# Kernel optimization log

Measured on AMD Instinct MI355X. Metric: run time of the kernel, lower is better.

Reference implementation:

```python
import jax, jax.numpy as jnp
import numpy as np

B, S, H = 4, 1024, 2048
NQ, NKV, D = 32, 4, 128
EPS = 1e-6
THETA = 1e6


def setup_inputs() -> dict:
    key = jax.random.key(0)
    k1, k2, k3 = jax.random.split(key, 3)
    hidden = jax.random.normal(k1, (B, S, H), jnp.float32) * 0.02
    w_qkv = jax.random.normal(k2, (H, (NQ + 2 * NKV) * D), jnp.float32) * 0.02
    w_o = jax.random.normal(k3, (NQ * D, H), jnp.float32) * 0.02
    q_norm_w = jnp.ones((D,), jnp.float32)
    k_norm_w = jnp.ones((D,), jnp.float32)
    # rotary tables, broadcast to [B, S, D]
    inv_freq = 1.0 / (THETA ** (jnp.arange(0, D, 2, dtype=jnp.float32) / D))
    freqs = jnp.arange(S, dtype=jnp.float32)[:, None] * inv_freq[None, :]  # [S, D/2]
    emb = jnp.concatenate([freqs, freqs], axis=-1)  # [S, D]
    cos = jnp.broadcast_to(jnp.cos(emb)[None], (B, S, D))
    sin = jnp.broadcast_to(jnp.sin(emb)[None], (B, S, D))
    return {"hidden": hidden, "w_qkv": w_qkv, "w_o": w_o,
            "q_norm_w": q_norm_w, "k_norm_w": k_norm_w, "cos": cos, "sin": sin}


def _rms_norm(x, w):
    xf = x.astype(jnp.float32)
    var = jnp.mean(xf * xf, axis=-1, keepdims=True)
    return (w * (xf * jax.lax.rsqrt(var + EPS))).astype(x.dtype)


def _rotate_half(x):
    h = x.shape[-1] // 2
    return jnp.concatenate([-x[..., h:], x[..., :h]], axis=-1)


def reference(hidden, w_qkv, w_o, q_norm_w, k_norm_w, cos, sin):
    b, s, _ = hidden.shape
    qkv = jnp.einsum('bsh,he->bse', hidden, w_qkv)
    q = qkv[..., : NQ * D].reshape(b, s, NQ, D)
    k = qkv[..., NQ * D: (NQ + NKV) * D].reshape(b, s, NKV, D)
    v = qkv[..., (NQ + NKV) * D:].reshape(b, s, NKV, D)

    # per-head RMSNorm on Q and K
    q = _rms_norm(q, q_norm_w)
    k = _rms_norm(k, k_norm_w)

    # fused RoPE (rotate-half), cos/sin broadcast over heads
    c = cos[:, :, None, :]
    sn = sin[:, :, None, :]
    q = q * c + _rotate_half(q) * sn
    k = k * c + _rotate_half(k) * sn

    # GQA causal flash-attention (prefill, sparse_mode=3 -> causal)
    g = NQ // NKV
    qg = q.reshape(b, s, NKV, g, D)
    scale = 1.0 / jnp.sqrt(jnp.asarray(D, hidden.dtype))
    scores = jnp.einsum('bqkgd,bskd->bkgqs', qg, k) * scale  # [B,NKV,g,S,S]
    causal = jnp.tril(jnp.ones((s, s), bool))
    scores = jnp.where(causal[None, None, None], scores, jnp.finfo(scores.dtype).min)
    probs = jax.nn.softmax(scores, axis=-1)
    out = jnp.einsum('bkgqs,bskd->bqkgd', probs, v).reshape(b, s, NQ * D)
    return jnp.einsum('bse,eh->bsh', out, w_o)
```

## Files before the change

### kernel.cpp

```cpp
#include <hip/hip_runtime.h>

#define BB 4
#define SS 1024
#define HH 2048
#define NQH 32
#define NKVH 4
#define DD 128
#define EQKV 5120

typedef __attribute__((ext_vector_type(8))) short s8v;
typedef __attribute__((ext_vector_type(4))) short s4v;
typedef __attribute__((ext_vector_type(4))) float f4v;

__device__ __forceinline__ unsigned short f2bf(float f) {
  unsigned int u = __builtin_bit_cast(unsigned int, f);
  u += 0x7fffu + ((u >> 16) & 1u);
  return (unsigned short)(u >> 16);
}
__device__ __forceinline__ float bf2f(unsigned short s) {
  unsigned int u = ((unsigned int)s) << 16;
  return __builtin_bit_cast(float, u);
}

__device__ __forceinline__ void async16(unsigned short* lds, const unsigned short* g) {
  __builtin_amdgcn_global_load_lds(
      (const __attribute__((address_space(1))) unsigned int*)g,
      (__attribute__((address_space(3))) unsigned int*)lds, 16, 0, 0);
}


__global__ __launch_bounds__(256) void cvt_bf16(const float* __restrict__ in,
                                                unsigned short* __restrict__ out, int n) {
  int i = (blockIdx.x * 256 + threadIdx.x) * 4;
  if (i >= n) return;
  f4v v = *reinterpret_cast<const f4v*>(in + i);
  s4v o;
#pragma unroll
  for (int j = 0; j < 4; ++j) o[j] = (short)f2bf(v[j]);
  *reinterpret_cast<s4v*>(out + i) = o;
}

__global__ __launch_bounds__(256) void transpose_cvt(const float* __restrict__ in,
                                                     unsigned short* __restrict__ out,
                                                     int K, int N) {
  __shared__ unsigned short T[64][65];
  const int k0 = blockIdx.y * 64, n0 = blockIdx.x * 64;
  const int t = threadIdx.x;
  const int r = t >> 4, c4 = (t & 15) * 4;
#pragma unroll
  for (int i = 0; i < 4; ++i) {
    f4v v = *reinterpret_cast<const f4v*>(&in[(size_t)(k0 + r + i * 16) * N + n0 + c4]);
#pragma unroll
    for (int j = 0; j < 4; ++j) T[r + i * 16][c4 + j] = f2bf(v[j]);
  }
  __syncthreads();
#pragma unroll
  for (int i = 0; i < 4; ++i) {
    int n = r + i * 16;
    s4v o;
#pragma unroll
    for (int j = 0; j < 4; ++j) o[j] = (short)T[c4 + j][n];
    *reinterpret_cast<s4v*>(&out[(size_t)(n0 + n) * K + k0 + c4]) = o;
  }
}

__global__ __launch_bounds__(256) void vtrans(const unsigned short* __restrict__ qkv,
                                              unsigned short* __restrict__ Vt) {
  __shared__ unsigned short T[64][68];
  const int s0 = blockIdx.x * 64;
  const int d0 = blockIdx.y * 64;
  const int bk = blockIdx.z;
  const int b = bk >> 2, hkv = bk & 3;
  const int t = threadIdx.x;
  const int r = t >> 4, c4 = (t & 15) * 4;
  const unsigned short* src = qkv + (size_t)(b * SS + s0) * EQKV + (NQH + NKVH + hkv) * DD + d0;
#pragma unroll
  for (int i = 0; i < 4; ++i) {
    int s = r + i * 16;
    s4v v = *reinterpret_cast<const s4v*>(src + (size_t)s * EQKV + c4);
    *reinterpret_cast<s4v*>(&T[s][c4]) = v;
  }
  __syncthreads();
#pragma unroll
  for (int i = 0; i < 4; ++i) {
    int d = r + i * 16;
    s4v o;
#pragma unroll
    for (int j = 0; j < 4; ++j) o[j] = (short)T[c4 + j][d];
    *reinterpret_cast<s4v*>(&Vt[((size_t)bk * DD + d0 + d) * SS + s0 + c4]) = o;
  }
}

template <bool CF32>
__global__ __launch_bounds__(512) void gemm_deep(const unsigned short* __restrict__ A,
                                                 const unsigned short* __restrict__ Bt,
                                                 void* __restrict__ Cp,
                                                 int M, int N, int K, int lda) {
  __shared__ unsigned short RING[6][12288];
  const int tid = threadIdx.x;
  const int ln = tid & 63, w = tid >> 6;
  const int la = ln & 15, quad = ln >> 4;
  const int wr = w >> 2, wc = w & 3;

  const int G = gridDim.x, cpx = G >> 3;
  const int swz = (blockIdx.x & 7) * cpx + (blockIdx.x >> 3);
  const int ytiles = M >> 7;
  const int by = swz % ytiles, bx = swz / ytiles;
  const int m0 = by * 128, n0 = bx * 256;

  f4v acc[4][4] = {};

  const int srow = tid >> 2;
  const int schunk = (tid & 3) ^ ((tid >> 3) & 3);
  const int rb0 = w * 32 + (ln >> 2);
  const unsigned short* pA  = A  + (size_t)(m0 + srow) * lda + schunk * 8;
  const unsigned short* pB0 = Bt + (size_t)(n0 + rb0) * K   + schunk * 8;
  const unsigned short* pB1 = pB0 + (size_t)16 * K;
  unsigned short* ldsA = nullptr;

  const int fch = (quad ^ ((la >> 1) & 3)) * 8;
  const int ar = (wr * 64 + la) * 32;
  const int br = 4096 + (wc * 64 + la) * 32;

#define STAGE(s, koff)                                          \
  async16(&RING[s][w * 512], pA + (koff));                      \
  async16(&RING[s][4096 + w * 1024], pB0 + (koff));             \
  async16(&RING[s][4096 + w * 1024 + 512], pB1 + (koff));

#pragma unroll
  for (int pp = 0; pp < 5; ++pp) { STAGE(pp, pp * 32) }
  asm volatile("s_waitcnt vmcnt(12)" ::: "memory");
  __builtin_amdgcn_s_barrier();

  const int NP = K >> 5;
  const int kend = K - 32;
  int u = 0, su = 5, ks = 160;
  for (int p = 0; p < NP; ++p) {
    s8v a0 = *reinterpret_cast<const s8v*>(&RING[u][ar + fch]);
    s8v a1 = *reinterpret_cast<const s8v*>(&RING[u][ar + 512 + fch]);
    s8v a2 = *reinterpret_cast<const s8v*>(&RING[u][ar + 1024 + fch]);
    s8v a3 = *reinterpret_cast<const s8v*>(&RING[u][ar + 1536 + fch]);
    s8v b0 = *reinterpret_cast<const s8v*>(&RING[u][br + fch]);
    s8v b1 = *reinterpret_cast<const s8v*>(&RING[u][br + 512 + fch]);
    s8v b2 = *reinterpret_cast<const s8v*>(&RING[u][br + 1024 + fch]);
    s8v b3 = *reinterpret_cast<const s8v*>(&RING[u][br + 1536 + fch]);
    STAGE(su, ks)
    __builtin_amdgcn_s_setprio(1);
    acc[0][0] = __builtin_amdgcn_mfma_f32_16x16x32_bf16(a0, b0, acc[0][0], 0, 0, 0);
    acc[0][1] = __builtin_amdgcn_mfma_f32_16x16x32_bf16(a0, b1, acc[0][1], 0, 0, 0);
    acc[0][2] = __builtin_amdgcn_mfma_f32_16x16x32_bf16(a0, b2, acc[0][2], 0, 0, 0);
    acc[0][3] = __builtin_amdgcn_mfma_f32_16x16x32_bf16(a0, b3, acc[0][3], 0, 0, 0);
    acc[1][0] = __builtin_amdgcn_mfma_f32_16x16x32_bf16(a1, b0, acc[1][0], 0, 0, 0);
    acc[1][1] = __builtin_amdgcn_mfma_f32_16x16x32_bf16(a1, b1, acc[1][1], 0, 0, 0);
    acc[1][2] = __builtin_amdgcn_mfma_f32_16x16x32_bf16(a1, b2, acc[1][2], 0, 0, 0);
    acc[1][3] = __builtin_amdgcn_mfma_f32_16x16x32_bf16(a1, b3, acc[1][3], 0, 0, 0);
    acc[2][0] = __builtin_amdgcn_mfma_f32_16x16x32_bf16(a2, b0, acc[2][0], 0, 0, 0);
    acc[2][1] = __builtin_amdgcn_mfma_f32_16x16x32_bf16(a2, b1, acc[2][1], 0, 0, 0);
    acc[2][2] = __builtin_amdgcn_mfma_f32_16x16x32_bf16(a2, b2, acc[2][2], 0, 0, 0);
    acc[2][3] = __builtin_amdgcn_mfma_f32_16x16x32_bf16(a2, b3, acc[2][3], 0, 0, 0);
    acc[3][0] = __builtin_amdgcn_mfma_f32_16x16x32_bf16(a3, b0, acc[3][0], 0, 0, 0);
    acc[3][1] = __builtin_amdgcn_mfma_f32_16x16x32_bf16(a3, b1, acc[3][1], 0, 0, 0);
    acc[3][2] = __builtin_amdgcn_mfma_f32_16x16x32_bf16(a3, b2, acc[3][2], 0, 0, 0);
    acc[3][3] = __builtin_amdgcn_mfma_f32_16x16x32_bf16(a3, b3, acc[3][3], 0, 0, 0);
    __builtin_amdgcn_s_setprio(0);
    asm volatile("s_waitcnt vmcnt(12)" ::: "memory");
    __builtin_amdgcn_s_barrier();
    u = (u == 5) ? 0 : u + 1;
    su = (su == 5) ? 0 : su + 1;
    ks = (ks < kend) ? ks + 32 : ks;
  }
  asm volatile("s_waitcnt vmcnt(0)" ::: "memory");
#undef STAGE

#pragma unroll
  for (int mf = 0; mf < 4; ++mf)
#pragma unroll
    for (int nf = 0; nf < 4; ++nf)
#pragma unroll
      for (int r = 0; r < 4; ++r) {
        int row = m0 + wr * 64 + mf * 16 + quad * 4 + r;
        int col = n0 + wc * 64 + nf * 16 + la;
        if constexpr (CF32) ((float*)Cp)[(size_t)row * N + col] = acc[mf][nf][r];
        else ((unsigned short*)Cp)[(size_t)row * N + col] = f2bf(acc[mf][nf][r]);
      }
}

__global__ __launch_bounds__(256) void attn2(unsigned short* __restrict__ qkv,
                                             const unsigned short* __restrict__ Vt) {
  const int idx = blockIdx.x;
  const int tile = 15 - (idx >> 7);
  const int h = idx & 31;
  const int b = (idx >> 5) & 3;
  const int hkv = h >> 3;
  const int tid = threadIdx.x;
  const int ln = tid & 63, w = tid >> 6;
  const int la = ln & 15, quad = ln >> 4;
  const int qr0 = tile * 64;
  __shared__ unsigned short Ks[64 * 128];
  __shared__ unsigned short Vts[128 * 64];
  __shared__ unsigned short Ps[4][16][64];

  const size_t rowb = (size_t)b * SS;
  s8v qf[4];
  {
    const unsigned short* qrow = qkv + (rowb + qr0 + w * 16 + la) * EQKV + h * DD;
#pragma unroll
    for (int t = 0; t < 4; ++t) qf[t] = *reinterpret_cast<const s8v*>(qrow + t * 32 + quad * 8);
  }
  const unsigned short* kcol = qkv + (NQH + hkv) * DD;
  const unsigned short* vtb = Vt + (size_t)(b * NKVH + hkv) * DD * SS;

  float m_[4], l_[4], al[4];
  f4v acc[8] = {};
#pragma unroll
  for (int r = 0; r < 4; ++r) { m_[r] = -1.0e30f; l_[r] = 0.f; }

  const float scale = 0.08838834764831845f;
  const int nkb = tile + 1;
  for (int kb = 0; kb < nkb; ++kb) {
    const int key0 = kb * 64;
    __syncthreads();
#pragma unroll
    for (int i = 0; i < 4; ++i) {
      int row = w * 16 + i * 4 + (ln >> 4);
      int chunk = (ln & 15) ^ (row & 15);
      async16(&Ks[(w * 16 + i * 4) * 128],
              kcol + (rowb + key0 + row) * EQKV + chunk * 8);
    }
#pragma unroll
    for (int i = 0; i < 4; ++i) {
      int row = w * 32 + i * 8 + (ln >> 3);
      int chunk = (ln & 7) ^ (ln >> 3);
      async16(&Vts[(w * 32 + i * 8) * 64],
              vtb + (size_t)row * SS + key0 + chunk * 8);
    }
    __syncthreads();
    f4v sc[4];
#pragma unroll
    for (int kt = 0; kt < 4; ++kt) {
      f4v z = {};
#pragma unroll
      for (int t = 0; t < 4; ++t) {
        s8v kf = *reinterpret_cast<const s8v*>(&Ks[(kt * 16 + la) * 128 + ((t * 4 + quad) ^ la) * 8]);
        z = __builtin_amdgcn_mfma_f32_16x16x32_bf16(qf[t], kf, z, 0, 0, 0);
      }
      sc[kt] = z;
    }
    const bool diag = (kb == nkb - 1);
#pragma unroll
    for (int r = 0; r < 4; ++r) {
      float v[4];
      if (diag) {
        int q = qr0 + w * 16 + quad * 4 + r;
#pragma unroll
        for (int kt = 0; kt < 4; ++kt)
          v[kt] = (key0 + kt * 16 + la <= q) ? sc[kt][r] * scale : -1.0e30f;
      } else {
#pragma unroll
        for (int kt = 0; kt < 4; ++kt) v[kt] = sc[kt][r] * scale;
      }
      float mx = fmaxf(fmaxf(v[0], v[1]), fmaxf(v[2], v[3]));
#pragma unroll
      for (int off = 8; off >= 1; off >>= 1) mx = fmaxf(mx, __shfl_xor(mx, off));
      float mnew = fmaxf(m_[r], mx);
      al[r] = __expf(m_[r] - mnew);
      m_[r] = mnew;
      float rsum = 0.f;
      const int row = quad * 4 + r;
#pragma unroll
      for (int kt = 0; kt < 4; ++kt) {
        float p = __expf(v[kt] - mnew);
        rsum += p;
        int col = kt * 16 + la;
        Ps[w][row][(((col >> 3) ^ (row & 7)) << 3) | (col & 7)] = f2bf(p);
      }
#pragma unroll
      for (int off = 8; off >= 1; off >>= 1) rsum += __shfl_xor(rsum, off);
      l_[r] = l_[r] * al[r] + rsum;
    }
#pragma unroll
    for (int nt = 0; nt < 8; ++nt)
#pragma unroll
      for (int r = 0; r < 4; ++r) acc[nt][r] *= al[r];
#pragma unroll
    for (int c = 0; c < 2; ++c) {
      s8v pf = *reinterpret_cast<const s8v*>(&Ps[w][la][(((c * 4 + quad) ^ (la & 7)) << 3)]);
#pragma unroll
      for (int nt = 0; nt < 8; ++nt) {
        s8v vf = *reinterpret_cast<const s8v*>(
            &Vts[(nt * 16 + la) * 64 + ((c * 4 + quad) ^ (la & 7)) * 8]);
        acc[nt] = __builtin_amdgcn_mfma_f32_16x16x32_bf16(pf, vf, acc[nt], 0, 0, 0);
      }
    }
  }
#pragma unroll
  for (int nt = 0; nt < 8; ++nt)
#pragma unroll
    for (int r = 0; r < 4; ++r) {
      int q = qr0 + w * 16 + quad * 4 + r;
      qkv[(rowb + q) * EQKV + h * DD + nt * 16 + la] = f2bf(acc[nt][r] / l_[r]);
    }
}

template <bool AF32, bool BF32, bool CF32>
__global__ __launch_bounds__(256) void gemm_t(const void* __restrict__ Ap,
                                              const void* __restrict__ Bp,
                                              void* __restrict__ Cp,
                                              int M, int N, int K, int lda) {
  __shared__ unsigned short As[64][40];
  __shared__ unsigned short Bs[64][40];
  const int tid  = threadIdx.x;
  const int lane = tid & 63;
  const int wave = tid >> 6;
  const int la   = lane & 15;
  const int quad = lane >> 4;
  const int m0 = blockIdx.y * 64;
  const int n0 = blockIdx.x * 64;
  const int wm = (wave >> 1) * 32;
  const int wn = (wave & 1) * 32;
  f4v acc[2][2] = {};
  const int ar = tid >> 2, ac = (tid & 3) * 8;
  const int bk = tid >> 3, bn = (tid & 7) * 8;
  for (int k0 = 0; k0 < K; k0 += 32) {
    s8v av;
    if constexpr (AF32) {
      const float* a = (const float*)Ap + (size_t)(m0 + ar) * lda + ac + k0;
      f4v v0 = *reinterpret_cast<const f4v*>(a);
      f4v v1 = *reinterpret_cast<const f4v*>(a + 4);
#pragma unroll
      for (int j = 0; j < 4; ++j) { av[j] = (short)f2bf(v0[j]); av[j + 4] = (short)f2bf(v1[j]); }
    } else {
      av = *reinterpret_cast<const s8v*>((const unsigned short*)Ap + (size_t)(m0 + ar) * lda + ac + k0);
    }
    unsigned short bvs[8];
    if constexpr (BF32) {
      const float* bp = (const float*)Bp + (size_t)(k0 + bk) * N + n0 + bn;
      f4v v0 = *reinterpret_cast<const f4v*>(bp);
      f4v v1 = *reinterpret_cast<const f4v*>(bp + 4);
#pragma unroll
      for (int j = 0; j < 4; ++j) { bvs[j] = f2bf(v0[j]); bvs[j + 4] = f2bf(v1[j]); }
    } else {
      s8v bv = *reinterpret_cast<const s8v*>((const unsigned short*)Bp + (size_t)(k0 + bk) * N + n0 + bn);
#pragma unroll
      for (int j = 0; j < 8; ++j) bvs[j] = (unsigned short)bv[j];
    }
    *reinterpret_cast<s8v*>(&As[ar][ac]) = av;
#pragma unroll
    for (int j = 0; j < 8; ++j) Bs[bn + j][bk] = bvs[j];
    __syncthreads();
#pragma unroll
    for (int mi = 0; mi < 2; ++mi) {
      s8v af = *reinterpret_cast<const s8v*>(&As[wm + mi * 16 + la][quad * 8]);
#pragma unroll
      for (int ni = 0; ni < 2; ++ni) {
        s8v bfr = *reinterpret_cast<const s8v*>(&Bs[wn + ni * 16 + la][quad * 8]);
        acc[mi][ni] = __builtin_amdgcn_mfma_f32_16x16x32_bf16(af, bfr, acc[mi][ni], 0, 0, 0);
      }
    }
    __syncthreads();
  }
#pragma unroll
  for (int mi = 0; mi < 2; ++mi)
#pragma unroll
    for (int ni = 0; ni < 2; ++ni)
#pragma unroll
      for (int r = 0; r < 4; ++r) {
        int row = m0 + wm + mi * 16 + quad * 4 + r;
        int col = n0 + wn + ni * 16 + la;
        if constexpr (CF32) ((float*)Cp)[(size_t)row * N + col] = acc[mi][ni][r];
        else ((unsigned short*)Cp)[(size_t)row * N + col] = f2bf(acc[mi][ni][r]);
      }
}

__global__ __launch_bounds__(64) void attn_slow(unsigned short* __restrict__ qkv) {
  const int tile = blockIdx.x;
  const int h = blockIdx.y;
  const int b = blockIdx.z;
  const int hkv = h >> 3;
  const int lane = threadIdx.x;
  const int la = lane & 15;
  const int quad = lane >> 4;
  const int qr0 = tile * 16;
  __shared__ unsigned short P[16][32];
  __shared__ unsigned short V[32][128];
  const size_t base = (size_t)b * SS * EQKV;
  s8v qf[4];
  {
    const unsigned short* qrow = qkv + base + (size_t)(qr0 + la) * EQKV + h * DD;
#pragma unroll
    for (int t = 0; t < 4; ++t)
      qf[t] = *reinterpret_cast<const s8v*>(qrow + t * 32 + quad * 8);
  }
  const unsigned short* kbase = qkv + base + (NQH + hkv) * DD;
  const unsigned short* vbase = qkv + base + (NQH + NKVH + hkv) * DD;
  float m[4], l[4], al[4];
  f4v acc[8] = {};
#pragma unroll
  for (int r = 0; r < 4; ++r) { m[r] = -1.0e30f; l[r] = 0.f; }
  const float scale = 0.08838834764831845f;
  const int nkb = (qr0 + 16 + 31) >> 5;
  for (int kb = 0; kb < nkb; ++kb) {
    const int key0 = kb * 32;
    __syncthreads();
#pragma unroll
    for (int i = 0; i < 8; ++i) {
      int c = i * 64 + lane;
      int row = c >> 4, col = (c & 15) * 8;
      *reinterpret_cast<s8v*>(&V[row][col]) =
          *reinterpret_cast<const s8v*>(vbase + (size_t)(key0 + row) * EQKV + col);
    }
    f4v s0 = {}, s1 = {};
#pragma unroll
    for (int t = 0; t < 4; ++t) {
      s8v k0f = *reinterpret_cast<const s8v*>(kbase + (size_t)(key0 + la) * EQKV + t * 32 + quad * 8);
      s8v k1f = *reinterpret_cast<const s8v*>(kbase + (size_t)(key0 + 16 + la) * EQKV + t * 32 + quad * 8);
      s0 = __builtin_amdgcn_mfma_f32_16x16x32_bf16(qf[t], k0f, s0, 0, 0, 0);
      s1 = __builtin_amdgcn_mfma_f32_16x16x32_bf16(qf[t], k1f, s1, 0, 0, 0);
    }
#pragma unroll
    for (int r = 0; r < 4; ++r) {
      int q = qr0 + quad * 4 + r;
      float v0 = (key0 + la <= q) ? s0[r] * scale : -1.0e30f;
      float v1 = (key0 + 16 + la <= q) ? s1[r] * scale : -1.0e30f;
      float mx = fmaxf(v0, v1);
#pragma unroll
      for (int off = 8; off >= 1; off >>= 1) mx = fmaxf(mx, __shfl_xor(mx, off));
      float mnew = fmaxf(m[r], mx);
      float p0 = __expf(v0 - mnew);
      float p1 = __expf(v1 - mnew);
      al[r] = __expf(m[r] - mnew);
      m[r] = mnew;
      float rsum = p0 + p1;
#pragma unroll
      for (int off = 8; off >= 1; off >>= 1) rsum += __shfl_xor(rsum, off);
      l[r] = l[r] * al[r] + rsum;
      P[quad * 4 + r][la] = f2bf(p0);
      P[quad * 4 + r][la + 16] = f2bf(p1);
    }
#pragma unroll
    for (int nt = 0; nt < 8; ++nt)
#pragma unroll
      for (int r = 0; r < 4; ++r) acc[nt][r] *= al[r];
    __syncthreads();
    s8v pf = *reinterpret_cast<const s8v*>(&P[la][quad * 8]);
#pragma unroll
    for (int nt = 0; nt < 8; ++nt) {
      s8v vf;
#pragma unroll
      for (int j = 0; j < 8; ++j)
        vf[j] = (short)V[quad * 8 + j][nt * 16 + la];
      acc[nt] = __builtin_amdgcn_mfma_f32_16x16x32_bf16(pf, vf, acc[nt], 0, 0, 0);
    }
  }
#pragma unroll
  for (int nt = 0; nt < 8; ++nt)
#pragma unroll
    for (int r = 0; r < 4; ++r) {
      int q = qr0 + quad * 4 + r;
      qkv[base + (size_t)q * EQKV + h * DD + nt * 16 + la] = f2bf(acc[nt][r] / l[r]);
    }
}

__global__ __launch_bounds__(256) void norm_rope(unsigned short* __restrict__ qkv,
                                                 const float* __restrict__ qw,
                                                 const float* __restrict__ kw,
                                                 const float* __restrict__ cosp,
                                                 const float* __restrict__ sinp) {
  const int h = blockIdx.x;
  const int bs = blockIdx.y * 4 + (threadIdx.x >> 6);
  const int s = bs & (SS - 1);
  const int lane = threadIdx.x & 63;
  const int d0 = lane * 2;
  unsigned short* p = qkv + (size_t)bs * EQKV + h * DD + d0;
  unsigned int u = *reinterpret_cast<const unsigned int*>(p);
  float x0 = bf2f((unsigned short)(u & 0xffff));
  float x1 = bf2f((unsigned short)(u >> 16));
  float ss = x0 * x0 + x1 * x1;
#pragma unroll
  for (int off = 32; off >= 1; off >>= 1) ss += __shfl_xor(ss, off);
  float rs = rsqrtf(ss * (1.0f / 128.0f) + 1e-6f);
  const float* w = (h < NQH) ? qw : kw;
  float n0 = x0 * rs * w[d0];
  float n1 = x1 * rs * w[d0 + 1];
  float o0 = __shfl_xor(n0, 32);
  float o1 = __shfl_xor(n1, 32);
  float r0 = (lane < 32) ? -o0 : o0;
  float r1 = (lane < 32) ? -o1 : o1;
  float c0 = cosp[(size_t)s * DD + d0], c1 = cosp[(size_t)s * DD + d0 + 1];
  float s0 = sinp[(size_t)s * DD + d0], s1 = sinp[(size_t)s * DD + d0 + 1];
  float y0 = n0 * c0 + r0 * s0;
  float y1 = n1 * c1 + r1 * s1;
  unsigned int outv = (unsigned int)f2bf(y0) | ((unsigned int)f2bf(y1) << 16);
  *reinterpret_cast<unsigned int*>(p) = outv;
}

extern "C" void kernel_launch(void* const* d_in, const int* in_sizes, int n_in,
                              void* d_out, int out_size, void* d_ws, size_t ws_size,
                              hipStream_t stream) {
  const float* hidden = (const float*)d_in[0];
  const float* w_qkv  = (const float*)d_in[1];
  const float* w_o    = (const float*)d_in[2];
  const float* q_w    = (const float*)d_in[3];
  const float* k_w    = (const float*)d_in[4];
  const float* cosp   = (const float*)d_in[5];
  const float* sinp   = (const float*)d_in[6];
  float* out = (float*)d_out;

  const int M = BB * SS;
  const size_t szHid  = (size_t)M * HH;
  const size_t szWqkv = (size_t)HH * EQKV;
  const size_t szWo   = (size_t)(NQH * DD) * HH;
  const size_t szQkv  = (size_t)M * EQKV;
  const size_t need = (szHid + szWqkv + szWo + szQkv) * sizeof(unsigned short);

  if (ws_size >= need) {
    unsigned short* hb16  = (unsigned short*)d_ws;
    unsigned short* wqkvT = hb16 + szHid;
    unsigned short* woT   = wqkvT + szWqkv;
    unsigned short* qkv   = woT + szWo;
    unsigned short* Vt    = hb16;

    cvt_bf16<<<(int)(szHid / 1024), 256, 0, stream>>>(hidden, hb16, (int)szHid);
    transpose_cvt<<<dim3(EQKV / 64, HH / 64), 256, 0, stream>>>(w_qkv, wqkvT, HH, EQKV);
    transpose_cvt<<<dim3(HH / 64, (NQH * DD) / 64), 256, 0, stream>>>(w_o, woT, NQH * DD, HH);

    gemm_deep<false><<<(EQKV / 256) * (M / 128), 512, 0, stream>>>(
        hb16, wqkvT, qkv, M, EQKV, HH, HH);
    vtrans<<<dim3(SS / 64, DD / 64, BB * NKVH), 256, 0, stream>>>(qkv, Vt);
    norm_rope<<<dim3(NQH + NKVH, M / 4), 256, 0, stream>>>(qkv, q_w, k_w, cosp, sinp);
    attn2<<<2048, 256, 0, stream>>>(qkv, Vt);
    gemm_deep<true><<<(HH / 256) * (M / 128), 512, 0, stream>>>(
        qkv, woT, out, M, HH, NQH * DD, EQKV);
  } else {
    unsigned short* qkvb = (unsigned short*)d_ws;
    for (int b = 0; b < BB; ++b) {
      const float* hb = hidden + (size_t)b * SS * HH;
      float* ob = out + (size_t)b * SS * HH;
      gemm_t<true, true, false><<<dim3(EQKV / 64, SS / 64), 256, 0, stream>>>(
          hb, w_qkv, qkvb, SS, EQKV, HH, HH);
      norm_rope<<<dim3(NQH + NKVH, SS / 4), 256, 0, stream>>>(qkvb, q_w, k_w, cosp, sinp);
      attn_slow<<<dim3(SS / 16, NQH, 1), 64, 0, stream>>>(qkvb);
      gemm_t<false, true, true><<<dim3(HH / 64, SS / 64), 256, 0, stream>>>(
          qkvb, w_o, ob, SS, HH, NQH * DD, EQKV);
    }
  }
}
```

Before: 468.3 us.

## Enlarge GEMM tile to 256x256 and add lazy rescaling in attention softmax

The GEMM kernel now computes a 256x256 output tile per block instead of 128x256, with 32 accumulators per wave and a 4-stage LDS ring instead of 6. This raises data reuse per loaded fragment and halves the number of A/B tile loads. The cost is more register pressure and a shallower prefetch pipeline. In attention, the softmax keeps the running max in unscaled units, skips the rescale of the accumulators unless any row's max grows by more than a threshold, and defers the row-sum cross-lane reduction to the end. This removes per-block shuffles and accumulator multiplies, at the risk of larger intermediate exponent ranges.

```diff
diff --git a/kernel.cpp b/kernel.cpp
--- a/kernel.cpp
+++ b/kernel.cpp
@@ -92,11 +92,11 @@
 }
 
 template <bool CF32>
-__global__ __launch_bounds__(512) void gemm_deep(const unsigned short* __restrict__ A,
-                                                 const unsigned short* __restrict__ Bt,
-                                                 void* __restrict__ Cp,
-                                                 int M, int N, int K, int lda) {
-  __shared__ unsigned short RING[6][12288];
+__global__ __launch_bounds__(512) void gemm_256(const unsigned short* __restrict__ A,
+                                                const unsigned short* __restrict__ Bt,
+                                                void* __restrict__ Cp,
+                                                int M, int N, int K, int lda) {
+  __shared__ unsigned short RING[4][16384];
   const int tid = threadIdx.x;
   const int ln = tid & 63, w = tid >> 6;
   const int la = ln & 15, quad = ln >> 4;
@@ -104,81 +104,70 @@
 
   const int G = gridDim.x, cpx = G >> 3;
   const int swz = (blockIdx.x & 7) * cpx + (blockIdx.x >> 3);
-  const int ytiles = M >> 7;
+  const int ytiles = M >> 8;
   const int by = swz % ytiles, bx = swz / ytiles;
-  const int m0 = by * 128, n0 = bx * 256;
-
-  f4v acc[4][4] = {};
-
-  const int srow = tid >> 2;
-  const int schunk = (tid & 3) ^ ((tid >> 3) & 3);
-  const int rb0 = w * 32 + (ln >> 2);
-  const unsigned short* pA  = A  + (size_t)(m0 + srow) * lda + schunk * 8;
-  const unsigned short* pB0 = Bt + (size_t)(n0 + rb0) * K   + schunk * 8;
+  const int m0 = by * 256, n0 = bx * 256;
+
+  f4v acc[8][4] = {};
+
+  const int srow = w * 32 + (ln >> 2);
+  const int schunk = (ln & 3) ^ ((ln >> 3) & 3);
+  const unsigned short* pA0 = A + (size_t)(m0 + srow) * lda + schunk * 8;
+  const unsigned short* pA1 = pA0 + (size_t)16 * lda;
+  const unsigned short* pB0 = Bt + (size_t)(n0 + srow) * K + schunk * 8;
   const unsigned short* pB1 = pB0 + (size_t)16 * K;
-  unsigned short* ldsA = nullptr;
 
   const int fch = (quad ^ ((la >> 1) & 3)) * 8;
-  const int ar = (wr * 64 + la) * 32;
-  const int br = 4096 + (wc * 64 + la) * 32;
-
-#define STAGE(s, koff)                                          \
-  async16(&RING[s][w * 512], pA + (koff));                      \
-  async16(&RING[s][4096 + w * 1024], pB0 + (koff));             \
-  async16(&RING[s][4096 + w * 1024 + 512], pB1 + (koff));
-
-#pragma unroll
-  for (int pp = 0; pp < 5; ++pp) { STAGE(pp, pp * 32) }
-  asm volatile("s_waitcnt vmcnt(12)" ::: "memory");
+  const int ar = (wr * 128 + la) * 32;
+  const int br = 8192 + (wc * 64 + la) * 32;
+
+#define STAGE(s, koff)                                   \
+  async16(&RING[s][w * 1024], pA0 + (koff));             \
+  async16(&RING[s][w * 1024 + 512], pA1 + (koff));       \
+  async16(&RING[s][8192 + w * 1024], pB0 + (koff));      \
+  async16(&RING[s][8192 + w * 1024 + 512], pB1 + (koff));
+
+  STAGE(0, 0)
+  STAGE(1, 32)
+  STAGE(2, 64)
+  asm volatile("s_waitcnt vmcnt(8)" ::: "memory");
   __builtin_amdgcn_s_barrier();
 
   const int NP = K >> 5;
   const int kend = K - 32;
-  int u = 0, su = 5, ks = 160;
+  int u = 0, ks = 96;
   for (int p = 0; p < NP; ++p) {
-    s8v a0 = *reinterpret_cast<const s8v*>(&RING[u][ar + fch]);
-    s8v a1 = *reinterpret_cast<const s8v*>(&RING[u][ar + 512 + fch]);
-    s8v a2 = *reinterpret_cast<const s8v*>(&RING[u][ar + 1024 + fch]);
-    s8v a3 = *reinterpret_cast<const s8v*>(&RING[u][ar + 1536 + fch]);
-    s8v b0 = *reinterpret_cast<const s8v*>(&RING[u][br + fch]);
-    s8v b1 = *reinterpret_cast<const s8v*>(&RING[u][br + 512 + fch]);
-    s8v b2 = *reinterpret_cast<const s8v*>(&RING[u][br + 1024 + fch]);
-    s8v b3 = *reinterpret_cast<const s8v*>(&RING[u][br + 1536 + fch]);
-    STAGE(su, ks)
+    s8v a[8], b[4];
+#pragma unroll
+    for (int mf = 0; mf < 8; ++mf)
+      a[mf] = *reinterpret_cast<const s8v*>(&RING[u][ar + mf * 512 + fch]);
+#pragma unroll
+    for (int nf = 0; nf < 4; ++nf)
+      b[nf] = *reinterpret_cast<const s8v*>(&RING[u][br + nf * 512 + fch]);
+    const int s3 = (u + 3) & 3;
+    STAGE(s3, ks)
     __builtin_amdgcn_s_setprio(1);
-    acc[0][0] = __builtin_amdgcn_mfma_f32_16x16x32_bf16(a0, b0, acc[0][0], 0, 0, 0);
-    acc[0][1] = __builtin_amdgcn_mfma_f32_16x16x32_bf16(a0, b1, acc[0][1], 0, 0, 0);
-    acc[0][2] = __builtin_amdgcn_mfma_f32_16x16x32_bf16(a0, b2, acc[0][2], 0, 0, 0);
-    acc[0][3] = __builtin_amdgcn_mfma_f32_16x16x32_bf16(a0, b3, acc[0][3], 0, 0, 0);
-    acc[1][0] = __builtin_amdgcn_mfma_f32_16x16x32_bf16(a1, b0, acc[1][0], 0, 0, 0);
-    acc[1][1] = __builtin_amdgcn_mfma_f32_16x16x32_bf16(a1, b1, acc[1][1], 0, 0, 0);
-    acc[1][2] = __builtin_amdgcn_mfma_f32_16x16x32_bf16(a1, b2, acc[1][2], 0, 0, 0);
-    acc[1][3] = __builtin_amdgcn_mfma_f32_16x16x32_bf16(a1, b3, acc[1][3], 0, 0, 0);
-    acc[2][0] = __builtin_amdgcn_mfma_f32_16x16x32_bf16(a2, b0, acc[2][0], 0, 0, 0);
-    acc[2][1] = __builtin_amdgcn_mfma_f32_16x16x32_bf16(a2, b1, acc[2][1], 0, 0, 0);
-    acc[2][2] = __builtin_amdgcn_mfma_f32_16x16x32_bf16(a2, b2, acc[2][2], 0, 0, 0);
-    acc[2][3] = __builtin_amdgcn_mfma_f32_16x16x32_bf16(a2, b3, acc[2][3], 0, 0, 0);
-    acc[3][0] = __builtin_amdgcn_mfma_f32_16x16x32_bf16(a3, b0, acc[3][0], 0, 0, 0);
-    acc[3][1] = __builtin_amdgcn_mfma_f32_16x16x32_bf16(a3, b1, acc[3][1], 0, 0, 0);
-    acc[3][2] = __builtin_amdgcn_mfma_f32_16x16x32_bf16(a3, b2, acc[3][2], 0, 0, 0);
-    acc[3][3] = __builtin_amdgcn_mfma_f32_16x16x32_bf16(a3, b3, acc[3][3], 0, 0, 0);
+#pragma unroll
+    for (int mf = 0; mf < 8; ++mf)
+#pragma unroll
+      for (int nf = 0; nf < 4; ++nf)
+        acc[mf][nf] = __builtin_amdgcn_mfma_f32_16x16x32_bf16(a[mf], b[nf], acc[mf][nf], 0, 0, 0);
     __builtin_amdgcn_s_setprio(0);
-    asm volatile("s_waitcnt vmcnt(12)" ::: "memory");
+    asm volatile("s_waitcnt vmcnt(8)" ::: "memory");
     __builtin_amdgcn_s_barrier();
-    u = (u == 5) ? 0 : u + 1;
-    su = (su == 5) ? 0 : su + 1;
+    u = (u + 1) & 3;
     ks = (ks < kend) ? ks + 32 : ks;
   }
   asm volatile("s_waitcnt vmcnt(0)" ::: "memory");
 #undef STAGE
 
 #pragma unroll
-  for (int mf = 0; mf < 4; ++mf)
+  for (int mf = 0; mf < 8; ++mf)
 #pragma unroll
     for (int nf = 0; nf < 4; ++nf)
 #pragma unroll
       for (int r = 0; r < 4; ++r) {
-        int row = m0 + wr * 64 + mf * 16 + quad * 4 + r;
+        int row = m0 + wr * 128 + mf * 16 + quad * 4 + r;
         int col = n0 + wc * 64 + nf * 16 + la;
         if constexpr (CF32) ((float*)Cp)[(size_t)row * N + col] = acc[mf][nf][r];
         else ((unsigned short*)Cp)[(size_t)row * N + col] = f2bf(acc[mf][nf][r]);
@@ -210,12 +199,12 @@
   const unsigned short* kcol = qkv + (NQH + hkv) * DD;
   const unsigned short* vtb = Vt + (size_t)(b * NKVH + hkv) * DD * SS;
 
-  float m_[4], l_[4], al[4];
+  float m_[4], ls[4];
   f4v acc[8] = {};
 #pragma unroll
-  for (int r = 0; r < 4; ++r) { m_[r] = -1.0e30f; l_[r] = 0.f; }
-
-  const float scale = 0.08838834764831845f;
+  for (int r = 0; r < 4; ++r) { m_[r] = -1.0e30f; ls[r] = 0.f; }
+
+  const float SC = 0.08838834764831845f;
   const int nkb = tile + 1;
   for (int kb = 0; kb < nkb; ++kb) {
     const int key0 = kb * 64;
@@ -247,41 +236,46 @@
       sc[kt] = z;
     }
     const bool diag = (kb == nkb - 1);
+    float pmax[4];
 #pragma unroll
     for (int r = 0; r < 4; ++r) {
-      float v[4];
       if (diag) {
         int q = qr0 + w * 16 + quad * 4 + r;
 #pragma unroll
         for (int kt = 0; kt < 4; ++kt)
-          v[kt] = (key0 + kt * 16 + la <= q) ? sc[kt][r] * scale : -1.0e30f;
-      } else {
-#pragma unroll
-        for (int kt = 0; kt < 4; ++kt) v[kt] = sc[kt][r] * scale;
-      }
-      float mx = fmaxf(fmaxf(v[0], v[1]), fmaxf(v[2], v[3]));
-#pragma unroll
-      for (int off = 8; off >= 1; off >>= 1) mx = fmaxf(mx, __shfl_xor(mx, off));
-      float mnew = fmaxf(m_[r], mx);
-      al[r] = __expf(m_[r] - mnew);
-      m_[r] = mnew;
-      float rsum = 0.f;
+          if (key0 + kt * 16 + la > q) sc[kt][r] = -1.0e30f;
+      }
+      pmax[r] = fmaxf(fmaxf(sc[0][r], sc[1][r]), fmaxf(sc[2][r], sc[3][r]));
+    }
+    int need = 0;
+#pragma unroll
+    for (int r = 0; r < 4; ++r) need |= (pmax[r] > m_[r] + 64.0f) ? 1 : 0;
+    if (__any(need)) {
+#pragma unroll
+      for (int r = 0; r < 4; ++r) {
+        float mx = pmax[r];
+#pragma unroll
+        for (int off = 8; off >= 1; off >>= 1) mx = fmaxf(mx, __shfl_xor(mx, off));
+        float mnew = fmaxf(m_[r], mx);
+        float al = __expf((m_[r] - mnew) * SC);
+        m_[r] = mnew;
+        ls[r] *= al;
+#pragma unroll
+        for (int nt = 0; nt < 8; ++nt) acc[nt][r] *= al;
+      }
+    }
+#pragma unroll
+    for (int r = 0; r < 4; ++r) {
       const int row = quad * 4 + r;
+      const float mS = m_[r] * SC;
 #pragma unroll
       for (int kt = 0; kt < 4; ++kt) {
-        float p = __expf(v[kt] - mnew);
-        rsum += p;
+        float p = __expf(__builtin_fmaf(sc[kt][r], SC, -mS));
+        ls[r] += p;
         int col = kt * 16 + la;
         Ps[w][row][(((col >> 3) ^ (row & 7)) << 3) | (col & 7)] = f2bf(p);
       }
-#pragma unroll
-      for (int off = 8; off >= 1; off >>= 1) rsum += __shfl_xor(rsum, off);
-      l_[r] = l_[r] * al[r] + rsum;
-    }
-#pragma unroll
-    for (int nt = 0; nt < 8; ++nt)
-#pragma unroll
-      for (int r = 0; r < 4; ++r) acc[nt][r] *= al[r];
+    }
 #pragma unroll
     for (int c = 0; c < 2; ++c) {
       s8v pf = *reinterpret_cast<const s8v*>(&Ps[w][la][(((c * 4 + quad) ^ (la & 7)) << 3)]);
@@ -294,11 +288,15 @@
     }
   }
 #pragma unroll
+  for (int r = 0; r < 4; ++r)
+#pragma unroll
+    for (int off = 8; off >= 1; off >>= 1) ls[r] += __shfl_xor(ls[r], off);
+#pragma unroll
   for (int nt = 0; nt < 8; ++nt)
 #pragma unroll
     for (int r = 0; r < 4; ++r) {
       int q = qr0 + w * 16 + quad * 4 + r;
-      qkv[(rowb + q) * EQKV + h * DD + nt * 16 + la] = f2bf(acc[nt][r] / l_[r]);
+      qkv[(rowb + q) * EQKV + h * DD + nt * 16 + la] = f2bf(acc[nt][r] / ls[r]);
     }
 }
 
@@ -524,12 +522,12 @@
     transpose_cvt<<<dim3(EQKV / 64, HH / 64), 256, 0, stream>>>(w_qkv, wqkvT, HH, EQKV);
     transpose_cvt<<<dim3(HH / 64, (NQH * DD) / 64), 256, 0, stream>>>(w_o, woT, NQH * DD, HH);
 
-    gemm_deep<false><<<(EQKV / 256) * (M / 128), 512, 0, stream>>>(
+    gemm_256<false><<<(M / 256) * (EQKV / 256), 512, 0, stream>>>(
         hb16, wqkvT, qkv, M, EQKV, HH, HH);
     vtrans<<<dim3(SS / 64, DD / 64, BB * NKVH), 256, 0, stream>>>(qkv, Vt);
     norm_rope<<<dim3(NQH + NKVH, M / 4), 256, 0, stream>>>(qkv, q_w, k_w, cosp, sinp);
     attn2<<<2048, 256, 0, stream>>>(qkv, Vt);
-    gemm_deep<true><<<(HH / 256) * (M / 128), 512, 0, stream>>>(
+    gemm_256<true><<<(M / 256) * (HH / 256), 512, 0, stream>>>(
         qkv, woT, out, M, HH, NQH * DD, EQKV);
   } else {
     unsigned short* qkvb = (unsigned short*)d_ws;
```

Result: faster. 454.7 us (-2.9%).
